# Kernel tuning notes

Hardware: AMD Instinct MI355X
Metric: run time of the kernel (lower is better)

## Reference

```python
import jax, jax.numpy as jnp
import numpy as np

KLD_SCALE = 10.0


def setup_inputs() -> dict:
    key = jax.random.key(0)
    k1, k2 = jax.random.split(key)
    B, C, H, W = 16, 64, 64, 64
    K = 1024
    inputs = jax.random.normal(k1, (B, C, H, W), dtype=jnp.float32)
    codebook = jax.random.normal(k2, (K, C), dtype=jnp.float32) * (1.0 / K)
    beta = jnp.float32(0.25)
    return {"inputs": inputs, "codebook": codebook, "beta": beta}


def reference(inputs, codebook, beta):
    # inputs: [B, C, H, W], codebook: [K, D] with D == C
    sg = jax.lax.stop_gradient
    x = jnp.transpose(inputs, (0, 2, 3, 1))          # [B, H, W, D]
    D = x.shape[-1]
    flat = x.reshape(-1, D)                           # [N, D]
    d = (jnp.sum(flat * flat, axis=1, keepdims=True)
         + jnp.sum(codebook * codebook, axis=1)
         - 2.0 * flat @ codebook.T)                   # [N, K]
    idx = jnp.argmin(d, axis=1)                       # [N]
    q = codebook[idx].reshape(x.shape)                # gather == one_hot @ codebook
    # training (non-EMA) loss: (beta*||q - sg(x)||^2 + ||sg(q) - x||^2) * kld_scale
    loss = beta * jnp.mean((q - sg(x)) ** 2)
    loss = (loss + jnp.mean((sg(q) - x) ** 2)) * KLD_SCALE
    # straight-through estimator
    q_st = x + sg(q - x)
    # perplexity from code usage histogram (== mean of one-hot rows)
    K = codebook.shape[0]
    counts = jnp.zeros((K,), dtype=flat.dtype).at[idx].add(1.0)
    e_mean = counts / flat.shape[0]
    perplexity = jnp.exp(-jnp.sum(e_mean * jnp.log(e_mean + 1e-10)))
    quantized = jnp.transpose(q_st, (0, 3, 1, 2))     # [B, C, H, W]
    return loss, quantized, perplexity
```

## Files before the change

kernel.cpp:

```cpp
#include <hip/hip_runtime.h>
#include <cfloat>

typedef __bf16 bf16x8 __attribute__((ext_vector_type(8)));
typedef float f32x16 __attribute__((ext_vector_type(16)));

namespace {
constexpr int kHW = 4096;
constexpr int kC = 64;
constexpr float kInvN = 1.0f / 65536.0f;


__global__ __launch_bounds__(64) void prep_kernel(
    const float* __restrict__ cb, uint4* __restrict__ frags,
    unsigned int* __restrict__ hist, float* __restrict__ lossacc) {
  const int c = blockIdx.x;
  const int l = threadIdx.x;
  const int lo = l & 31, hi = l >> 5;
  const int code = c * 32 + lo;

  #pragma unroll
  for (int ks = 0; ks < 4; ++ks) {
    bf16x8 fh, fl;
    #pragma unroll
    for (int e = 0; e < 8; ++e) {
      const int d = ks * 16 + hi * 8 + e;
      float v = -2.0f * cb[code * kC + d];
      __bf16 h = (__bf16)v;
      fh[e] = h;
      fl[e] = (__bf16)(v - (float)h);
    }
    frags[(c * 9 + ks) * 64 + l] = *reinterpret_cast<uint4*>(&fh);
    frags[(c * 9 + 4 + ks) * 64 + l] = *reinterpret_cast<uint4*>(&fl);
  }
  bf16x8 fb;
  #pragma unroll
  for (int e = 0; e < 8; ++e) fb[e] = (__bf16)0.0f;
  if (hi == 0) {
    float s = 0.0f;
    #pragma unroll
    for (int d = 0; d < kC; d += 4) {
      float4 v = *reinterpret_cast<const float4*>(cb + code * kC + d);
      s = fmaf(v.x, v.x, fmaf(v.y, v.y, fmaf(v.z, v.z, fmaf(v.w, v.w, s))));
    }
    __bf16 h = (__bf16)s;
    fb[0] = h;
    fb[1] = (__bf16)(s - (float)h);
    hist[code] = 0u;
  }
  frags[(c * 9 + 8) * 64 + l] = *reinterpret_cast<uint4*>(&fb);
  if (c == 0 && l == 0) lossacc[0] = 0.0f;
}

__global__ __launch_bounds__(256) void vq_kernel(
    const float* __restrict__ in, const bf16x8* __restrict__ frags,
    const float* __restrict__ cb, unsigned int* __restrict__ hist,
    float* __restrict__ lossacc, float* __restrict__ qout) {
  __shared__ int sIdx[128];
  const int t = threadIdx.x;
  const int lane = t & 63, wv = t >> 6;
  const int lo = lane & 31, hi = lane >> 5;
  const int site = blockIdx.x * 128 + wv * 32 + lo;
  const int b = site >> 12, hw = site & 4095;
  const float* xp = in + b * (kC * kHW) + hw;

  bf16x8 Bh[4], Bl[4];
  #pragma unroll
  for (int ks = 0; ks < 4; ++ks) {
    #pragma unroll
    for (int e = 0; e < 8; ++e) {
      const int d = ks * 16 + hi * 8 + e;
      float v = xp[d * kHW];
      __bf16 h = (__bf16)v;
      Bh[ks][e] = h;
      Bl[ks][e] = (__bf16)(v - (float)h);
    }
  }
  bf16x8 ones;
  #pragma unroll
  for (int e = 0; e < 8; ++e) ones[e] = (__bf16)0.0f;
  if (hi == 0) { ones[0] = (__bf16)1.0f; ones[1] = (__bf16)1.0f; }
  f32x16 zero;
  #pragma unroll
  for (int r = 0; r < 16; ++r) zero[r] = 0.0f;

  float best[16];
  int bch[16];
  #pragma unroll
  for (int r = 0; r < 16; ++r) { best[r] = FLT_MAX; bch[r] = 0; }

  const bf16x8* fA = frags + lane;

  bf16x8 A0[9], A1[9];
  auto prefetch = [&](bf16x8(&F)[9], int c) {
    #pragma unroll
    for (int j = 0; j < 9; ++j) F[j] = fA[(c * 9 + j) * 64];
  };
  auto compute = [&](const bf16x8(&F)[9], int c) {
    f32x16 a1 = __builtin_amdgcn_mfma_f32_32x32x16_bf16(F[8], ones, zero, 0, 0, 0);
    f32x16 a2 = zero;
    #pragma unroll
    for (int ks = 0; ks < 4; ++ks) {
      a1 = __builtin_amdgcn_mfma_f32_32x32x16_bf16(F[ks], Bh[ks], a1, 0, 0, 0);
      a2 = __builtin_amdgcn_mfma_f32_32x32x16_bf16(F[4 + ks], Bh[ks], a2, 0, 0, 0);
      a2 = __builtin_amdgcn_mfma_f32_32x32x16_bf16(F[ks], Bl[ks], a2, 0, 0, 0);
    }
    #pragma unroll
    for (int r = 0; r < 16; ++r) {
      float d = a1[r] + a2[r];
      bool p = d < best[r];
      best[r] = p ? d : best[r];
      bch[r] = p ? c : bch[r];
    }
  };

  prefetch(A0, 0);
  #pragma unroll 1
  for (int c = 0; c < 32; c += 2) {
    prefetch(A1, c + 1);
    compute(A0, c);
    if (c + 2 < 32) prefetch(A0, c + 2);
    compute(A1, c + 1);
  }

  float bv = best[0];
  int bidx = bch[0] * 32 + (hi << 2);
  #pragma unroll
  for (int r = 1; r < 16; ++r) {
    const int kloc = (r & 3) + 8 * (r >> 2) + (hi << 2);
    int idx = bch[r] * 32 + kloc;
    float v = best[r];
    if (v < bv || (v == bv && idx < bidx)) { bv = v; bidx = idx; }
  }
  float ov = __shfl_xor(bv, 32, 64);
  int oi = __shfl_xor(bidx, 32, 64);
  if (ov < bv || (ov == bv && oi < bidx)) { bv = ov; bidx = oi; }
  if (hi == 0) {
    sIdx[wv * 32 + lo] = bidx;
    atomicAdd(&hist[bidx], 1u);
  }
  __syncthreads();

  {
    const int s2 = t & 127;
    const int dbase = (t >> 7) * 32;
    const int gsite = blockIdx.x * 128 + s2;
    const int b2 = gsite >> 12, hw2 = gsite & 4095;
    const int code = sIdx[s2];
    const float* xr = in + b2 * (kC * kHW) + hw2;
    const float* qr = cb + code * kC + dbase;
    float* op = qout + b2 * (kC * kHW) + hw2;
    float ls = 0.0f;
    #pragma unroll
    for (int j = 0; j < 32; j += 4) {
      float4 qv = *reinterpret_cast<const float4*>(qr + j);
      float q[4] = {qv.x, qv.y, qv.z, qv.w};
      #pragma unroll
      for (int u = 0; u < 4; ++u) {
        const int d = dbase + j + u;
        float xv = xr[d * kHW];
        float diff = q[u] - xv;
        ls = fmaf(diff, diff, ls);
        op[d * kHW] = xv + diff;
      }
    }
    #pragma unroll
    for (int off = 32; off; off >>= 1) ls += __shfl_xor(ls, off, 64);
    if (lane == 0) atomicAdd(lossacc, ls);
  }
}

__global__ __launch_bounds__(1024) void finalize_kernel(
    const unsigned int* __restrict__ hist, const float* __restrict__ lossacc,
    const float* __restrict__ beta, float* __restrict__ out) {
  __shared__ float red[16];
  const int t = threadIdx.x;
  float e = (float)hist[t] * kInvN;
  float term = e * logf(e + 1e-10f);
  #pragma unroll
  for (int off = 32; off; off >>= 1) term += __shfl_xor(term, off, 64);
  if ((t & 63) == 0) red[t >> 6] = term;
  __syncthreads();
  if (t == 0) {
    float h = 0.0f;
    #pragma unroll
    for (int i = 0; i < 16; ++i) h += red[i];
    out[1 + 4194304] = expf(-h);
    out[0] = lossacc[0] * (1.0f + beta[0]) * 10.0f / 4194304.0f;
  }
}
}

extern "C" void kernel_launch(void* const* d_in, const int* in_sizes, int n_in,
                              void* d_out, int out_size, void* d_ws, size_t ws_size,
                              hipStream_t stream) {
  const float* inputs = (const float*)d_in[0];
  const float* cb = (const float*)d_in[1];
  const float* beta = (const float*)d_in[2];
  float* out = (float*)d_out;

  uint4* frags = (uint4*)d_ws;
  unsigned int* hist = (unsigned int*)((char*)d_ws + 294912);
  float* lossacc = (float*)((char*)d_ws + 294912 + 4096);

  prep_kernel<<<32, 64, 0, stream>>>(cb, frags, hist, lossacc);
  vq_kernel<<<512, 256, 0, stream>>>(inputs, (const bf16x8*)frags, cb, hist,
                                     lossacc, out + 1);
  finalize_kernel<<<1, 1024, 0, stream>>>(hist, lossacc, beta, out);
}
```

Baseline: 127.5 us.

## Split codebook search across wave pairs and widen prep kernel parallelism

Each VQ block now handles 64 sites, with two waves per site group each scanning half of the codebook. Their argmins are merged through shared memory, and the grid doubles to 1024 blocks to give more parallelism and occupancy (launch bounds now set a minimum of 4 blocks). The hi/lo MFMA split accumulators are fused into a single serial accumulator chain, which lengthens the dependency chain but saves registers. The prep kernel also spreads the four k-slices across four waves with vectorized loads. The cost is an extra barrier and a shared-memory reduction, and each block re-loads its inputs for twice as many blocks.

Result: slower. 258.6 us (+102.8%).

```diff
diff --git a/kernel.cpp b/kernel.cpp
--- a/kernel.cpp
+++ b/kernel.cpp
@@ -10,56 +10,64 @@
 constexpr float kInvN = 1.0f / 65536.0f;
 
 
-__global__ __launch_bounds__(64) void prep_kernel(
+__global__ __launch_bounds__(256) void prep_kernel(
     const float* __restrict__ cb, uint4* __restrict__ frags,
     unsigned int* __restrict__ hist, float* __restrict__ lossacc) {
   const int c = blockIdx.x;
-  const int l = threadIdx.x;
-  const int lo = l & 31, hi = l >> 5;
+  const int t = threadIdx.x;
+  const int lane = t & 63, wv = t >> 6;
+  const int lo = lane & 31, hi = lane >> 5;
   const int code = c * 32 + lo;
-
-  #pragma unroll
-  for (int ks = 0; ks < 4; ++ks) {
-    bf16x8 fh, fl;
-    #pragma unroll
-    for (int e = 0; e < 8; ++e) {
-      const int d = ks * 16 + hi * 8 + e;
-      float v = -2.0f * cb[code * kC + d];
-      __bf16 h = (__bf16)v;
-      fh[e] = h;
-      fl[e] = (__bf16)(v - (float)h);
-    }
-    frags[(c * 9 + ks) * 64 + l] = *reinterpret_cast<uint4*>(&fh);
-    frags[(c * 9 + 4 + ks) * 64 + l] = *reinterpret_cast<uint4*>(&fl);
-  }
-  bf16x8 fb;
-  #pragma unroll
-  for (int e = 0; e < 8; ++e) fb[e] = (__bf16)0.0f;
-  if (hi == 0) {
-    float s = 0.0f;
-    #pragma unroll
-    for (int d = 0; d < kC; d += 4) {
-      float4 v = *reinterpret_cast<const float4*>(cb + code * kC + d);
-      s = fmaf(v.x, v.x, fmaf(v.y, v.y, fmaf(v.z, v.z, fmaf(v.w, v.w, s))));
-    }
-    __bf16 h = (__bf16)s;
-    fb[0] = h;
-    fb[1] = (__bf16)(s - (float)h);
-    hist[code] = 0u;
-  }
-  frags[(c * 9 + 8) * 64 + l] = *reinterpret_cast<uint4*>(&fb);
-  if (c == 0 && l == 0) lossacc[0] = 0.0f;
-}
-
-__global__ __launch_bounds__(256) void vq_kernel(
+  const int ks = wv;
+
+  const float* row = cb + code * kC + ks * 16 + hi * 8;
+  float4 v0 = *reinterpret_cast<const float4*>(row);
+  float4 v1 = *reinterpret_cast<const float4*>(row + 4);
+  float vv[8] = {v0.x, v0.y, v0.z, v0.w, v1.x, v1.y, v1.z, v1.w};
+  bf16x8 fh, fl;
+  #pragma unroll
+  for (int e = 0; e < 8; ++e) {
+    float v = -2.0f * vv[e];
+    __bf16 h = (__bf16)v;
+    fh[e] = h;
+    fl[e] = (__bf16)(v - (float)h);
+  }
+  frags[(c * 9 + ks) * 64 + lane] = *reinterpret_cast<uint4*>(&fh);
+  frags[(c * 9 + 4 + ks) * 64 + lane] = *reinterpret_cast<uint4*>(&fl);
+
+  if (wv == 0) {
+    bf16x8 fb;
+    #pragma unroll
+    for (int e = 0; e < 8; ++e) fb[e] = (__bf16)0.0f;
+    if (hi == 0) {
+      float s = 0.0f;
+      #pragma unroll
+      for (int d = 0; d < kC; d += 4) {
+        float4 v = *reinterpret_cast<const float4*>(cb + code * kC + d);
+        s = fmaf(v.x, v.x, fmaf(v.y, v.y, fmaf(v.z, v.z, fmaf(v.w, v.w, s))));
+      }
+      __bf16 h = (__bf16)s;
+      fb[0] = h;
+      fb[1] = (__bf16)(s - (float)h);
+    }
+    frags[(c * 9 + 8) * 64 + lane] = *reinterpret_cast<uint4*>(&fb);
+  }
+  if (t < 32) hist[c * 32 + t] = 0u;
+  if (c == 0 && t == 0) lossacc[0] = 0.0f;
+}
+
+__global__ __launch_bounds__(256, 4) void vq_kernel(
     const float* __restrict__ in, const bf16x8* __restrict__ frags,
     const float* __restrict__ cb, unsigned int* __restrict__ hist,
     float* __restrict__ lossacc, float* __restrict__ qout) {
-  __shared__ int sIdx[128];
+  __shared__ float sVal[4][32];
+  __shared__ int sIdxW[4][32];
+  __shared__ int sIdx[64];
   const int t = threadIdx.x;
   const int lane = t & 63, wv = t >> 6;
   const int lo = lane & 31, hi = lane >> 5;
-  const int site = blockIdx.x * 128 + wv * 32 + lo;
+  const int sg2 = wv & 1, kh = wv >> 1;
+  const int site = blockIdx.x * 64 + sg2 * 32 + lo;
   const int b = site >> 12, hw = site & 4095;
   const float* xp = in + b * (kC * kHW) + hw;
 
@@ -96,29 +104,31 @@
     for (int j = 0; j < 9; ++j) F[j] = fA[(c * 9 + j) * 64];
   };
   auto compute = [&](const bf16x8(&F)[9], int c) {
-    f32x16 a1 = __builtin_amdgcn_mfma_f32_32x32x16_bf16(F[8], ones, zero, 0, 0, 0);
-    f32x16 a2 = zero;
-    #pragma unroll
-    for (int ks = 0; ks < 4; ++ks) {
-      a1 = __builtin_amdgcn_mfma_f32_32x32x16_bf16(F[ks], Bh[ks], a1, 0, 0, 0);
-      a2 = __builtin_amdgcn_mfma_f32_32x32x16_bf16(F[4 + ks], Bh[ks], a2, 0, 0, 0);
-      a2 = __builtin_amdgcn_mfma_f32_32x32x16_bf16(F[ks], Bl[ks], a2, 0, 0, 0);
-    }
+    f32x16 a = __builtin_amdgcn_mfma_f32_32x32x16_bf16(F[8], ones, zero, 0, 0, 0);
+    #pragma unroll
+    for (int ks = 0; ks < 4; ++ks)
+      a = __builtin_amdgcn_mfma_f32_32x32x16_bf16(F[ks], Bh[ks], a, 0, 0, 0);
+    #pragma unroll
+    for (int ks = 0; ks < 4; ++ks)
+      a = __builtin_amdgcn_mfma_f32_32x32x16_bf16(F[4 + ks], Bh[ks], a, 0, 0, 0);
+    #pragma unroll
+    for (int ks = 0; ks < 4; ++ks)
+      a = __builtin_amdgcn_mfma_f32_32x32x16_bf16(F[ks], Bl[ks], a, 0, 0, 0);
     #pragma unroll
     for (int r = 0; r < 16; ++r) {
-      float d = a1[r] + a2[r];
-      bool p = d < best[r];
-      best[r] = p ? d : best[r];
+      bool p = a[r] < best[r];
+      best[r] = p ? a[r] : best[r];
       bch[r] = p ? c : bch[r];
     }
   };
 
-  prefetch(A0, 0);
+  const int c0 = kh * 16;
+  prefetch(A0, c0);
   #pragma unroll 1
-  for (int c = 0; c < 32; c += 2) {
+  for (int c = c0; c < c0 + 16; c += 2) {
     prefetch(A1, c + 1);
     compute(A0, c);
-    if (c + 2 < 32) prefetch(A0, c + 2);
+    if (c + 2 < c0 + 16) prefetch(A0, c + 2);
     compute(A1, c + 1);
   }
 
@@ -135,15 +145,23 @@
   int oi = __shfl_xor(bidx, 32, 64);
   if (ov < bv || (ov == bv && oi < bidx)) { bv = ov; bidx = oi; }
   if (hi == 0) {
-    sIdx[wv * 32 + lo] = bidx;
+    sVal[wv][lo] = bv;
+    sIdxW[wv][lo] = bidx;
+  }
+  __syncthreads();
+  if (wv < 2 && hi == 0) {
+    float v2 = sVal[wv + 2][lo];
+    int i2 = sIdxW[wv + 2][lo];
+    if (v2 < bv || (v2 == bv && i2 < bidx)) { bv = v2; bidx = i2; }
+    sIdx[sg2 * 32 + lo] = bidx;
     atomicAdd(&hist[bidx], 1u);
   }
   __syncthreads();
 
   {
-    const int s2 = t & 127;
-    const int dbase = (t >> 7) * 32;
-    const int gsite = blockIdx.x * 128 + s2;
+    const int s2 = t & 63;
+    const int dbase = (t >> 6) * 16;
+    const int gsite = blockIdx.x * 64 + s2;
     const int b2 = gsite >> 12, hw2 = gsite & 4095;
     const int code = sIdx[s2];
     const float* xr = in + b2 * (kC * kHW) + hw2;
@@ -151,7 +169,7 @@
     float* op = qout + b2 * (kC * kHW) + hw2;
     float ls = 0.0f;
     #pragma unroll
-    for (int j = 0; j < 32; j += 4) {
+    for (int j = 0; j < 16; j += 4) {
       float4 qv = *reinterpret_cast<const float4*>(qr + j);
       float q[4] = {qv.x, qv.y, qv.z, qv.w};
       #pragma unroll
@@ -202,8 +220,8 @@
   unsigned int* hist = (unsigned int*)((char*)d_ws + 294912);
   float* lossacc = (float*)((char*)d_ws + 294912 + 4096);
 
-  prep_kernel<<<32, 64, 0, stream>>>(cb, frags, hist, lossacc);
-  vq_kernel<<<512, 256, 0, stream>>>(inputs, (const bf16x8*)frags, cb, hist,
-                                     lossacc, out + 1);
+  prep_kernel<<<32, 256, 0, stream>>>(cb, (uint4*)frags, hist, lossacc);
+  vq_kernel<<<1024, 256, 0, stream>>>(inputs, (const bf16x8*)d_ws, cb, hist,
+                                      lossacc, out + 1);
   finalize_kernel<<<1, 1024, 0, stream>>>(hist, lossacc, beta, out);
 }
```
